# Kernel tuning notes

Measured on AMD Instinct MI355X. Metric: run time of the kernel, lower is better.

## Reference

```python
import jax, jax.numpy as jnp
import numpy as np

# Static pyramid shapes (H, W) per level; must match setup_inputs().
SPATIAL_SHAPES = [(128, 128), (64, 64), (32, 32), (16, 16)]
N, LQ, D_MODEL, M, L, P = 2, 21760, 256, 8, 4, 4
D_HEAD = D_MODEL // M
LEN_IN = sum(h * w for h, w in SPATIAL_SHAPES)


def _bilinear_sample(v, grid, H, W):
    """torch.grid_sample(mode=bilinear, padding=zeros, align_corners=False).
    v: [B, H, W, D], grid: [B, Q, P, 2] (x, y) in [-1, 1] -> [B, Q, P, D]."""
    gx = (grid[..., 0] + 1.0) * (W * 0.5) - 0.5
    gy = (grid[..., 1] + 1.0) * (H * 0.5) - 0.5
    x0 = jnp.floor(gx)
    y0 = jnp.floor(gy)
    wx1 = gx - x0
    wy1 = gy - y0
    b = jnp.arange(v.shape[0])[:, None, None]

    def gather(yi, xi):
        valid = (xi >= 0) & (xi <= W - 1) & (yi >= 0) & (yi <= H - 1)
        xc = jnp.clip(xi, 0, W - 1).astype(jnp.int32)
        yc = jnp.clip(yi, 0, H - 1).astype(jnp.int32)
        return v[b, yc, xc] * valid[..., None].astype(v.dtype)

    return (gather(y0, x0) * ((1 - wy1) * (1 - wx1))[..., None]
            + gather(y0, x0 + 1) * ((1 - wy1) * wx1)[..., None]
            + gather(y0 + 1, x0) * (wy1 * (1 - wx1))[..., None]
            + gather(y0 + 1, x0 + 1) * (wy1 * wx1)[..., None])


def setup_inputs() -> dict:
    key = jax.random.key(0)
    ks = jax.random.split(key, 12)
    s = 0.02
    return {
        "query": jax.random.normal(ks[0], (N, LQ, D_MODEL), jnp.float32),
        "reference_points": jax.random.uniform(ks[1], (N, LQ, L, 2), jnp.float32),
        "value": jax.random.normal(ks[2], (N, LEN_IN, D_MODEL), jnp.float32),
        "value_spatial_shapes": jnp.array(SPATIAL_SHAPES, jnp.int32),
        "W_val": jax.random.normal(ks[3], (D_MODEL, D_MODEL), jnp.float32) * s,
        "b_val": jnp.zeros((D_MODEL,), jnp.float32),
        "W_off": jax.random.normal(ks[4], (D_MODEL, M * L * P * 2), jnp.float32) * s,
        "b_off": jax.random.normal(ks[5], (M * L * P * 2,), jnp.float32) * s,
        "W_attn": jax.random.normal(ks[6], (D_MODEL, M * L * P), jnp.float32) * s,
        "b_attn": jnp.zeros((M * L * P,), jnp.float32),
        "W_out": jax.random.normal(ks[7], (D_MODEL, D_MODEL), jnp.float32) * s,
        "b_out": jnp.zeros((D_MODEL,), jnp.float32),
    }


def reference(query, reference_points, value, value_spatial_shapes,
              W_val, b_val, W_off, b_off, W_attn, b_attn, W_out, b_out):
    # value_spatial_shapes is treated as static (SPATIAL_SHAPES) for jit safety.
    v = (value @ W_val + b_val).reshape(N, LEN_IN, M, D_HEAD)
    off = (query @ W_off + b_off).reshape(N, LQ, M, L, P, 2)
    aw = jax.nn.softmax((query @ W_attn + b_attn).reshape(N, LQ, M, L * P), axis=-1)
    aw = aw.reshape(N, LQ, M, L, P)
    # normalizer stacks (W, H) -> x normalized by W, y by H
    norm = jnp.array([[w, h] for h, w in SPATIAL_SHAPES], dtype=query.dtype)
    loc = reference_points[:, :, None, :, None, :] + off / norm[None, None, None, :, None, :]
    grid = 2.0 * loc - 1.0  # [N, LQ, M, L, P, 2]

    out = jnp.zeros((N * M, LQ, D_HEAD), query.dtype)
    start = 0
    for lid, (H, W) in enumerate(SPATIAL_SHAPES):
        vl = v[:, start:start + H * W].reshape(N, H, W, M, D_HEAD)
        vl = vl.transpose(0, 3, 1, 2, 4).reshape(N * M, H, W, D_HEAD)
        gl = grid[:, :, :, lid].transpose(0, 2, 1, 3, 4).reshape(N * M, LQ, P, 2)
        sl = _bilinear_sample(vl, gl, H, W)  # [N*M, LQ, P, D]
        wl = aw[:, :, :, lid].transpose(0, 2, 1, 3).reshape(N * M, LQ, P)
        out = out + jnp.einsum('bqpd,bqp->bqd', sl, wl)
        start += H * W

    out = out.reshape(N, M, LQ, D_HEAD).transpose(0, 2, 1, 3).reshape(N, LQ, D_MODEL)
    return out @ W_out + b_out
```

## Files before the change

### kernel.cpp

```cpp
#include <hip/hip_runtime.h>

typedef __attribute__((ext_vector_type(8))) short short8;
typedef __attribute__((ext_vector_type(4))) float floatx4;

#define N_    2
#define LQ_   21760
#define D_    256
#define M_    8
#define L_    4
#define P_    4
#define DH_   32
#define LEN_  21760
#define BQ    16

__constant__ int c_start[4] = {0, 16384, 20480, 21504};
__constant__ int c_HW[4]    = {128, 64, 32, 16};

#define WT_BYTE_OFF 22282240u

__device__ __forceinline__ unsigned short f2bf(float f) {
  unsigned int u = __builtin_bit_cast(unsigned int, f);
  u += 0x7fffu + ((u >> 16) & 1u);
  return (unsigned short)(u >> 16);
}
__device__ __forceinline__ float bf2f(unsigned short s) {
  return __builtin_bit_cast(float, ((unsigned int)s) << 16);
}
__device__ __forceinline__ float bflo(unsigned int u) {
  return __builtin_bit_cast(float, u << 16);
}
__device__ __forceinline__ float bfhi(unsigned int u) {
  return __builtin_bit_cast(float, u & 0xffff0000u);
}

__global__ __launch_bounds__(256) void prep_kernel(
    const float* __restrict__ Woff, const float* __restrict__ Watt,
    const float* __restrict__ Wout, const float* __restrict__ Wv,
    unsigned short* __restrict__ wt) {
  const int b = blockIdx.x, t = threadIdx.x;
  const float* src; int ncols, n; unsigned short* dst;
  if (b < 256)      { src = Woff; ncols = 256; n = b;       dst = wt + 0      + n * 256; }
  else if (b < 384) { src = Watt; ncols = 128; n = b - 256; dst = wt + 65536  + n * 256; }
  else if (b < 640) { src = Wout; ncols = 256; n = b - 384; dst = wt + 98304  + n * 256; }
  else              { src = Wv;   ncols = 256; n = b - 640; dst = wt + 163840 + n * 256; }
  dst[t] = f2bf(src[(size_t)t * ncols + n]);
}

__global__ __launch_bounds__(256, 2) void vproj_kernel(
    const float* __restrict__ value, const unsigned short* __restrict__ Wvt,
    const float* __restrict__ bv, unsigned short* __restrict__ vout) {
  __shared__ unsigned short vs[64][264];
  const int t = threadIdx.x;
  const int r0 = blockIdx.x * 64;
  {
    const int c2 = (t & 127) * 2;
    const int rb = t >> 7;
#pragma unroll
    for (int i = 0; i < 32; ++i) {
      int rr = rb + i * 2;
      float2 v = *(const float2*)(value + (size_t)(r0 + rr) * D_ + c2);
      *(unsigned int*)&vs[rr][c2] = (unsigned int)f2bf(v.x) | ((unsigned int)f2bf(v.y) << 16);
    }
  }
  __syncthreads();
  const int wave = t >> 6, lane = t & 63;
  const int arow = wave * 16 + (lane & 15);
  const int kg = (lane >> 4) * 8;
  floatx4 acc[16] = {};
  for (int kk = 0; kk < 8; ++kk) {
    const int k0 = kk * 32;
    short8 af = *(const short8*)&vs[arow][k0 + kg];
#pragma unroll
    for (int ct = 0; ct < 16; ++ct) {
      const int col = ct * 16 + (lane & 15);
      short8 bf = *(const short8*)(Wvt + col * 256 + k0 + kg);
      acc[ct] = __builtin_amdgcn_mfma_f32_16x16x32_bf16(af, bf, acc[ct], 0, 0, 0);
    }
  }
  const int n = (r0 >= LEN_) ? 1 : 0;
  const int pixbase = r0 - n * LEN_ + wave * 16 + ((lane >> 4) * 4);
#pragma unroll
  for (int ct = 0; ct < 16; ++ct) {
    const int gc = ct * 16 + (lane & 15);
    const int m = gc >> 5, d = gc & 31;
    const float bb = bv[gc];
    unsigned short* ob = vout + ((size_t)(n * M_ + m) * LEN_) * DH_ + d;
#pragma unroll
    for (int j = 0; j < 4; ++j)
      ob[(size_t)(pixbase + j) * DH_] = f2bf(acc[ct][j] + bb);
  }
}

__global__ __launch_bounds__(256, 5)
__attribute__((amdgpu_waves_per_eu(4, 5)))
void msda_kernel(
    const float* __restrict__ query, const float* __restrict__ refp,
    const unsigned short* __restrict__ wt,
    const float* __restrict__ boff, const float* __restrict__ batt,
    const float* __restrict__ bout,
    const unsigned short* __restrict__ vproj, float* __restrict__ out) {
  __shared__ unsigned short qs[BQ][264];
  __shared__ unsigned short offb[BQ][256];
  __shared__ float awb[BQ][128];
  __shared__ short sidx[4][2][2][16];
  __shared__ float swls[4][2][2][16][4];

  const int t = threadIdx.x;
  const int lb = (blockIdx.x & 7) * 340 + (blockIdx.x >> 3);
  const int qg0 = lb * BQ;
  const int n = qg0 / LQ_;

  {
    const int c2 = (t & 127) * 2;
    const int rb = t >> 7;
#pragma unroll
    for (int i = 0; i < 8; ++i) {
      int rr = rb + i * 2;
      float2 v = *(const float2*)(query + (size_t)(qg0 + rr) * D_ + c2);
      *(unsigned int*)&qs[rr][c2] = (unsigned int)f2bf(v.x) | ((unsigned int)f2bf(v.y) << 16);
    }
  }
  __syncthreads();

  const int wave = t >> 6, lane = t & 63;
  const int arow = lane & 15;
  const int kg = (lane >> 4) * 8;
  const int row0 = (lane >> 4) * 4;

  {
    floatx4 acc[6] = {};
    for (int kk = 0; kk < 8; ++kk) {
      const int k0 = kk * 32;
      short8 af = *(const short8*)&qs[arow][k0 + kg];
#pragma unroll
      for (int i = 0; i < 6; ++i) {
        const int col = wave * 96 + i * 16 + (lane & 15);
        const unsigned short* bp = (col < 256) ? (wt + col * 256)
                                               : (wt + 65536 + (col - 256) * 256);
        short8 bf = *(const short8*)(bp + k0 + kg);
        acc[i] = __builtin_amdgcn_mfma_f32_16x16x32_bf16(af, bf, acc[i], 0, 0, 0);
      }
    }
#pragma unroll
    for (int i = 0; i < 6; ++i) {
      const int col = wave * 96 + i * 16 + (lane & 15);
      if (col < 256) {
        const float bb = boff[col];
#pragma unroll
        for (int j = 0; j < 4; ++j) offb[row0 + j][col] = f2bf(acc[i][j] + bb);
      } else {
        const float bb = batt[col - 256];
#pragma unroll
        for (int j = 0; j < 4; ++j) awb[row0 + j][col - 256] = acc[i][j] + bb;
      }
    }
  }
  __syncthreads();

  if (t < 128) {
    const int q = t >> 3, m = t & 7;
    float v[16]; float mx = -1e30f;
#pragma unroll
    for (int s = 0; s < 16; ++s) { v[s] = awb[q][m * 16 + s]; mx = fmaxf(mx, v[s]); }
    float sum = 0.f;
#pragma unroll
    for (int s = 0; s < 16; ++s) { v[s] = __expf(v[s] - mx); sum += v[s]; }
    const float inv = 1.f / sum;
#pragma unroll
    for (int s = 0; s < 16; ++s) awb[q][m * 16 + s] = v[s] * inv;
  }
  __syncthreads();

  const int qo  = lane >> 5;
  const int sh  = (lane >> 4) & 1;
  const int ss  = lane & 15;
  const int slv = ss >> 2;
  const int WlS = 128 >> slv;
  const int stS = c_start[slv];
  const int st_eq = (2 * wave + sh) * 16 + ss;
  const int hg = lane >> 5;
  const int m_g = 2 * wave + hg;
  const int g = lane & 31;
  const int sp = g >> 4, rsel = (g >> 3) & 1, csel = (g >> 2) & 1;
  const int wsel = (g >> 2) & 3, doct = g & 3;
  const char* vbyte = (const char*)vproj + (size_t)(n * M_ + m_g) * LEN_ * DH_ * 2;

  const float2* refp2 = (const float2*)refp;
  float2 rp[8];
#pragma unroll
  for (int e = 0; e < 8; ++e)
    rp[e] = refp2[(size_t)(qg0 + 2 * e + qo) * 4 + slv];

  for (int e = 0; e < 8; ++e) {
    {
      const int q = 2 * e + qo;
      const float gx = rp[e].x * (float)WlS + bf2f(offb[q][2 * st_eq])     - 0.5f;
      const float gy = rp[e].y * (float)WlS + bf2f(offb[q][2 * st_eq + 1]) - 0.5f;
      const float fx0 = floorf(gx), fy0 = floorf(gy);
      const int x0 = (int)fx0, y0 = (int)fy0;
      const float wx1 = gx - fx0, wy1 = gy - fy0;
      const float wx0 = 1.f - wx1, wy0 = 1.f - wy1;
      const float a = awb[q][st_eq];
      const bool vx0 = (x0 >= 0) && (x0 < WlS);
      const bool vx1 = (x0 + 1 >= 0) && (x0 + 1 < WlS);
      const bool vy0 = (y0 >= 0) && (y0 < WlS);
      const bool vy1 = (y0 + 1 >= 0) && (y0 + 1 < WlS);
      sidx[wave][qo][sh][ss] = (short)(stS + y0 * WlS + x0);
      swls[wave][qo][sh][ss][0] = (vy0 && vx0) ? wy0 * wx0 * a : 0.f;
      swls[wave][qo][sh][ss][1] = (vy0 && vx1) ? wy0 * wx1 * a : 0.f;
      swls[wave][qo][sh][ss][2] = (vy1 && vx0) ? wy1 * wx0 * a : 0.f;
      swls[wave][qo][sh][ss][3] = (vy1 && vx1) ? wy1 * wx1 * a : 0.f;
    }

#pragma unroll
    for (int qo2 = 0; qo2 < 2; ++qo2) {
      const int qp = 2 * e + qo2;
      uint4 u0, u1, u2, u3, u4, u5, u6, u7;
      float w0, w1, w2, w3, w4, w5, w6, w7;
#define GLD(i, WLC)                                                        \
      {                                                                    \
        const int s_ = 2 * (i) + sp;                                       \
        const int ix_ = (int)sidx[wave][qo2][hg][s_];                      \
        w##i = swls[wave][qo2][hg][s_][wsel];                              \
        int ofs_ = (ix_ + rsel * (WLC) + csel) * 64 + doct * 16;           \
        ofs_ = (ofs_ > 0) ? ofs_ : 0;                                      \
        u##i = *(const uint4*)(vbyte + ofs_);                              \
      }
      GLD(0, 128) GLD(1, 128) GLD(2, 64) GLD(3, 64)
      GLD(4, 32)  GLD(5, 32)  GLD(6, 16) GLD(7, 16)
#undef GLD

      float acc0 = 0.f, acc1 = 0.f, acc2 = 0.f, acc3 = 0.f;
      float acc4 = 0.f, acc5 = 0.f, acc6 = 0.f, acc7 = 0.f;
#define FMA8(i)                                                            \
      acc0 += bflo(u##i.x) * w##i; acc1 += bfhi(u##i.x) * w##i;            \
      acc2 += bflo(u##i.y) * w##i; acc3 += bfhi(u##i.y) * w##i;            \
      acc4 += bflo(u##i.z) * w##i; acc5 += bfhi(u##i.z) * w##i;            \
      acc6 += bflo(u##i.w) * w##i; acc7 += bfhi(u##i.w) * w##i;
      FMA8(0) FMA8(1) FMA8(2) FMA8(3) FMA8(4) FMA8(5) FMA8(6) FMA8(7)
#undef FMA8

      acc0 += __shfl_xor(acc0, 4);  acc1 += __shfl_xor(acc1, 4);
      acc2 += __shfl_xor(acc2, 4);  acc3 += __shfl_xor(acc3, 4);
      acc4 += __shfl_xor(acc4, 4);  acc5 += __shfl_xor(acc5, 4);
      acc6 += __shfl_xor(acc6, 4);  acc7 += __shfl_xor(acc7, 4);
      acc0 += __shfl_xor(acc0, 8);  acc1 += __shfl_xor(acc1, 8);
      acc2 += __shfl_xor(acc2, 8);  acc3 += __shfl_xor(acc3, 8);
      acc4 += __shfl_xor(acc4, 8);  acc5 += __shfl_xor(acc5, 8);
      acc6 += __shfl_xor(acc6, 8);  acc7 += __shfl_xor(acc7, 8);
      acc0 += __shfl_xor(acc0, 16); acc1 += __shfl_xor(acc1, 16);
      acc2 += __shfl_xor(acc2, 16); acc3 += __shfl_xor(acc3, 16);
      acc4 += __shfl_xor(acc4, 16); acc5 += __shfl_xor(acc5, 16);
      acc6 += __shfl_xor(acc6, 16); acc7 += __shfl_xor(acc7, 16);

      if (g < 4) {
        uint4 st4;
        st4.x = (unsigned int)f2bf(acc0) | ((unsigned int)f2bf(acc1) << 16);
        st4.y = (unsigned int)f2bf(acc2) | ((unsigned int)f2bf(acc3) << 16);
        st4.z = (unsigned int)f2bf(acc4) | ((unsigned int)f2bf(acc5) << 16);
        st4.w = (unsigned int)f2bf(acc6) | ((unsigned int)f2bf(acc7) << 16);
        *(uint4*)&qs[qp][m_g * 32 + doct * 8] = st4;
      }
    }
  }
  __syncthreads();

  {
    floatx4 acc[4] = {};
    for (int kk = 0; kk < 8; ++kk) {
      const int k0 = kk * 32;
      short8 af = *(const short8*)&qs[arow][k0 + kg];
#pragma unroll
      for (int i = 0; i < 4; ++i) {
        const int col = wave * 64 + i * 16 + (lane & 15);
        short8 bf = *(const short8*)(wt + 98304 + col * 256 + k0 + kg);
        acc[i] = __builtin_amdgcn_mfma_f32_16x16x32_bf16(af, bf, acc[i], 0, 0, 0);
      }
    }
#pragma unroll
    for (int i = 0; i < 4; ++i) {
      const int col = wave * 64 + i * 16 + (lane & 15);
      const float bb = bout[col];
#pragma unroll
      for (int j = 0; j < 4; ++j)
        out[(size_t)(qg0 + row0 + j) * D_ + col] = acc[i][j] + bb;
    }
  }
}

extern "C" void kernel_launch(void* const* d_in, const int* in_sizes, int n_in,
                              void* d_out, int out_size, void* d_ws, size_t ws_size,
                              hipStream_t stream) {
  const float* query = (const float*)d_in[0];
  const float* refp  = (const float*)d_in[1];
  const float* value = (const float*)d_in[2];
  const float* Wv    = (const float*)d_in[4];
  const float* bv    = (const float*)d_in[5];
  const float* Woff  = (const float*)d_in[6];
  const float* boff  = (const float*)d_in[7];
  const float* Watt  = (const float*)d_in[8];
  const float* batt  = (const float*)d_in[9];
  const float* Wout  = (const float*)d_in[10];
  const float* bout  = (const float*)d_in[11];
  float* out = (float*)d_out;

  unsigned short* vproj = (unsigned short*)d_ws;
  unsigned short* wt    = (unsigned short*)((char*)d_ws + WT_BYTE_OFF);
  const unsigned short* Wvt = wt + 163840;

  dim3 blk(256);
  hipLaunchKernelGGL(prep_kernel, dim3(896), blk, 0, stream, Woff, Watt, Wout, Wv, wt);
  hipLaunchKernelGGL(vproj_kernel, dim3((N_ * LEN_) / 64), blk, 0, stream, value, Wvt, bv, vproj);
  hipLaunchKernelGGL(msda_kernel, dim3((N_ * LQ_) / BQ), blk, 0, stream,
                     query, refp, wt, boff, batt, bout, vproj, out);
}
```

Baseline: 232.6 us.

## Split fused MSDA into per-head sampling kernel and separate output GEMM

Replaces the single fused msda kernel with two kernels when workspace allows. The first handles one (batch, head) pair per block over 64 queries, computing offsets and attention for that head only. Blocks are ordered by XCD so that each XCD's L2 cache serves a single head's value slice. It writes a bf16 intermediate, which a second MFMA kernel then multiplies by W_out. This aims for better cache locality in the gather, at the cost of an extra global round trip for the intermediate and one more launch.

```diff
diff --git a/kernel.cpp b/kernel.cpp
--- a/kernel.cpp
+++ b/kernel.cpp
@@ -17,6 +17,8 @@
 __constant__ int c_HW[4]    = {128, 64, 32, 16};
 
 #define WT_BYTE_OFF 22282240u
+#define MID_BYTE_OFF 22740992u
+#define WS_NEED_SPLIT 45023232ull
 
 __device__ __forceinline__ unsigned short f2bf(float f) {
   unsigned int u = __builtin_bit_cast(unsigned int, f);
@@ -88,6 +90,194 @@
 #pragma unroll
     for (int j = 0; j < 4; ++j)
       ob[(size_t)(pixbase + j) * DH_] = f2bf(acc[ct][j] + bb);
+  }
+}
+
+__global__ __launch_bounds__(256) void sample_kernel(
+    const float* __restrict__ query, const float* __restrict__ refp,
+    const unsigned short* __restrict__ wt,
+    const float* __restrict__ boff, const float* __restrict__ batt,
+    const unsigned short* __restrict__ vproj, unsigned short* __restrict__ mid) {
+  __shared__ unsigned short offh[64][34];
+  __shared__ float awh[64][17];
+  __shared__ short sidx[64][16];
+  __shared__ float swl[64][16][4];
+
+  const int t = threadIdx.x;
+  const int xcd = blockIdx.x & 7;
+  const int j = blockIdx.x >> 3;
+  const int pair = (j < 340) ? xcd : (8 + xcd);
+  const int qc = (j < 340) ? j : (j - 340);
+  const int n = pair >> 3, m = pair & 7;
+  const int q0 = qc * 64;
+  const size_t qrow0 = (size_t)n * LQ_ + q0;
+
+  const int wave = t >> 6, lane = t & 63;
+
+  {
+    const float* qptr = query + (qrow0 + wave * 16 + (lane & 15)) * D_;
+    floatx4 acc[3] = {};
+    for (int kk = 0; kk < 8; ++kk) {
+      const int k0 = kk * 32 + (lane >> 4) * 8;
+      float4 f0 = *(const float4*)(qptr + k0);
+      float4 f1 = *(const float4*)(qptr + k0 + 4);
+      short8 af;
+      af[0] = (short)f2bf(f0.x); af[1] = (short)f2bf(f0.y);
+      af[2] = (short)f2bf(f0.z); af[3] = (short)f2bf(f0.w);
+      af[4] = (short)f2bf(f1.x); af[5] = (short)f2bf(f1.y);
+      af[6] = (short)f2bf(f1.z); af[7] = (short)f2bf(f1.w);
+#pragma unroll
+      for (int i = 0; i < 3; ++i) {
+        const int lc = i * 16 + (lane & 15);
+        const unsigned short* bp = (lc < 32)
+            ? (wt + (m * 32 + lc) * 256)
+            : (wt + 65536 + (m * 16 + (lc - 32)) * 256);
+        short8 bf = *(const short8*)(bp + kk * 32 + (lane >> 4) * 8);
+        acc[i] = __builtin_amdgcn_mfma_f32_16x16x32_bf16(af, bf, acc[i], 0, 0, 0);
+      }
+    }
+    const int rw = wave * 16 + (lane >> 4) * 4;
+#pragma unroll
+    for (int i = 0; i < 3; ++i) {
+      const int lc = i * 16 + (lane & 15);
+      if (lc < 32) {
+        const float bb = boff[m * 32 + lc];
+#pragma unroll
+        for (int jj = 0; jj < 4; ++jj) offh[rw + jj][lc] = f2bf(acc[i][jj] + bb);
+      } else {
+        const float bb = batt[m * 16 + (lc - 32)];
+#pragma unroll
+        for (int jj = 0; jj < 4; ++jj) awh[rw + jj][lc - 32] = acc[i][jj] + bb;
+      }
+    }
+  }
+  __syncthreads();
+
+  if (t < 64) {
+    float v[16]; float mx = -1e30f;
+#pragma unroll
+    for (int s = 0; s < 16; ++s) { v[s] = awh[t][s]; mx = fmaxf(mx, v[s]); }
+    float sum = 0.f;
+#pragma unroll
+    for (int s = 0; s < 16; ++s) { v[s] = __expf(v[s] - mx); sum += v[s]; }
+    const float inv = 1.f / sum;
+#pragma unroll
+    for (int s = 0; s < 16; ++s) awh[t][s] = v[s] * inv;
+  }
+  __syncthreads();
+
+  {
+    const int q = t >> 2;
+    const int l = t & 3;
+    const int Wl = 128 >> l;
+    const int st = c_start[l];
+    const float2 rpv = *(const float2*)(refp + ((qrow0 + q) * 4 + l) * 2);
+#pragma unroll
+    for (int jj = 0; jj < 4; ++jj) {
+      const int s = l * 4 + jj;
+      const float gx = rpv.x * (float)Wl + bf2f(offh[q][2 * s])     - 0.5f;
+      const float gy = rpv.y * (float)Wl + bf2f(offh[q][2 * s + 1]) - 0.5f;
+      const float fx0 = floorf(gx), fy0 = floorf(gy);
+      const int x0 = (int)fx0, y0 = (int)fy0;
+      const float wx1 = gx - fx0, wy1 = gy - fy0;
+      const float wx0 = 1.f - wx1, wy0 = 1.f - wy1;
+      const float a = awh[q][s];
+      const bool vx0 = (x0 >= 0) && (x0 < Wl);
+      const bool vx1 = (x0 + 1 >= 0) && (x0 + 1 < Wl);
+      const bool vy0 = (y0 >= 0) && (y0 < Wl);
+      const bool vy1 = (y0 + 1 >= 0) && (y0 + 1 < Wl);
+      sidx[q][s] = (short)(st + y0 * Wl + x0);
+      swl[q][s][0] = (vy0 && vx0) ? wy0 * wx0 * a : 0.f;
+      swl[q][s][1] = (vy0 && vx1) ? wy0 * wx1 * a : 0.f;
+      swl[q][s][2] = (vy1 && vx0) ? wy1 * wx0 * a : 0.f;
+      swl[q][s][3] = (vy1 && vx1) ? wy1 * wx1 * a : 0.f;
+    }
+  }
+  __syncthreads();
+
+  const int qo = lane >> 5;
+  const int g = lane & 31;
+  const int sp = g >> 4, rsel = (g >> 3) & 1, csel = (g >> 2) & 1;
+  const int wsel = (g >> 2) & 3, doct = g & 3;
+  const char* vbyte = (const char*)vproj + (size_t)(n * M_ + m) * LEN_ * DH_ * 2;
+
+  for (int it = 0; it < 8; ++it) {
+    const int q = wave * 16 + it * 2 + qo;
+    uint4 u0, u1, u2, u3, u4, u5, u6, u7;
+    float w0, w1, w2, w3, w4, w5, w6, w7;
+#define GLD(i, WLC)                                                        \
+    {                                                                      \
+      const int s_ = 2 * (i) + sp;                                         \
+      const int ix_ = (int)sidx[q][s_];                                    \
+      w##i = swl[q][s_][wsel];                                             \
+      int ofs_ = (ix_ + rsel * (WLC) + csel) * 64 + doct * 16;             \
+      ofs_ = (ofs_ > 0) ? ofs_ : 0;                                        \
+      u##i = *(const uint4*)(vbyte + ofs_);                                \
+    }
+    GLD(0, 128) GLD(1, 128) GLD(2, 64) GLD(3, 64)
+    GLD(4, 32)  GLD(5, 32)  GLD(6, 16) GLD(7, 16)
+#undef GLD
+
+    float acc0 = 0.f, acc1 = 0.f, acc2 = 0.f, acc3 = 0.f;
+    float acc4 = 0.f, acc5 = 0.f, acc6 = 0.f, acc7 = 0.f;
+#define FMA8(i)                                                            \
+    acc0 += bflo(u##i.x) * w##i; acc1 += bfhi(u##i.x) * w##i;              \
+    acc2 += bflo(u##i.y) * w##i; acc3 += bfhi(u##i.y) * w##i;              \
+    acc4 += bflo(u##i.z) * w##i; acc5 += bfhi(u##i.z) * w##i;              \
+    acc6 += bflo(u##i.w) * w##i; acc7 += bfhi(u##i.w) * w##i;
+    FMA8(0) FMA8(1) FMA8(2) FMA8(3) FMA8(4) FMA8(5) FMA8(6) FMA8(7)
+#undef FMA8
+
+    acc0 += __shfl_xor(acc0, 4);  acc1 += __shfl_xor(acc1, 4);
+    acc2 += __shfl_xor(acc2, 4);  acc3 += __shfl_xor(acc3, 4);
+    acc4 += __shfl_xor(acc4, 4);  acc5 += __shfl_xor(acc5, 4);
+    acc6 += __shfl_xor(acc6, 4);  acc7 += __shfl_xor(acc7, 4);
+    acc0 += __shfl_xor(acc0, 8);  acc1 += __shfl_xor(acc1, 8);
+    acc2 += __shfl_xor(acc2, 8);  acc3 += __shfl_xor(acc3, 8);
+    acc4 += __shfl_xor(acc4, 8);  acc5 += __shfl_xor(acc5, 8);
+    acc6 += __shfl_xor(acc6, 8);  acc7 += __shfl_xor(acc7, 8);
+    acc0 += __shfl_xor(acc0, 16); acc1 += __shfl_xor(acc1, 16);
+    acc2 += __shfl_xor(acc2, 16); acc3 += __shfl_xor(acc3, 16);
+    acc4 += __shfl_xor(acc4, 16); acc5 += __shfl_xor(acc5, 16);
+    acc6 += __shfl_xor(acc6, 16); acc7 += __shfl_xor(acc7, 16);
+
+    if (g < 4) {
+      uint4 st4;
+      st4.x = (unsigned int)f2bf(acc0) | ((unsigned int)f2bf(acc1) << 16);
+      st4.y = (unsigned int)f2bf(acc2) | ((unsigned int)f2bf(acc3) << 16);
+      st4.z = (unsigned int)f2bf(acc4) | ((unsigned int)f2bf(acc5) << 16);
+      st4.w = (unsigned int)f2bf(acc6) | ((unsigned int)f2bf(acc7) << 16);
+      *(uint4*)(mid + ((qrow0 + q) * 8 + m) * 32 + doct * 8) = st4;
+    }
+  }
+}
+
+__global__ __launch_bounds__(256, 2) void outgemm_kernel(
+    const unsigned short* __restrict__ mid, const unsigned short* __restrict__ wtout,
+    const float* __restrict__ bout, float* __restrict__ out) {
+  const int t = threadIdx.x;
+  const int r0 = blockIdx.x * 64;
+  const int wave = t >> 6, lane = t & 63;
+  const int arow = r0 + wave * 16 + (lane & 15);
+  const int kg = (lane >> 4) * 8;
+  floatx4 acc[16] = {};
+  for (int kk = 0; kk < 8; ++kk) {
+    short8 af = *(const short8*)(mid + (size_t)arow * 256 + kk * 32 + kg);
+#pragma unroll
+    for (int ct = 0; ct < 16; ++ct) {
+      const int col = ct * 16 + (lane & 15);
+      short8 bf = *(const short8*)(wtout + col * 256 + kk * 32 + kg);
+      acc[ct] = __builtin_amdgcn_mfma_f32_16x16x32_bf16(af, bf, acc[ct], 0, 0, 0);
+    }
+  }
+  const int rwb = r0 + wave * 16 + (lane >> 4) * 4;
+#pragma unroll
+  for (int ct = 0; ct < 16; ++ct) {
+    const int col = ct * 16 + (lane & 15);
+    const float bb = bout[col];
+#pragma unroll
+    for (int jd = 0; jd < 4; ++jd)
+      out[(size_t)(rwb + jd) * D_ + col] = acc[ct][jd] + bb;
   }
 }
 
@@ -311,6 +501,15 @@
   dim3 blk(256);
   hipLaunchKernelGGL(prep_kernel, dim3(896), blk, 0, stream, Woff, Watt, Wout, Wv, wt);
   hipLaunchKernelGGL(vproj_kernel, dim3((N_ * LEN_) / 64), blk, 0, stream, value, Wvt, bv, vproj);
-  hipLaunchKernelGGL(msda_kernel, dim3((N_ * LQ_) / BQ), blk, 0, stream,
-                     query, refp, wt, boff, batt, bout, vproj, out);
-}
+
+  if (ws_size >= WS_NEED_SPLIT) {
+    unsigned short* mid = (unsigned short*)((char*)d_ws + MID_BYTE_OFF);
+    hipLaunchKernelGGL(sample_kernel, dim3(5440), blk, 0, stream,
+                       query, refp, wt, boff, batt, vproj, mid);
+    hipLaunchKernelGGL(outgemm_kernel, dim3((N_ * LQ_) / 64), blk, 0, stream,
+                       mid, wt + 98304, bout, out);
+  } else {
+    hipLaunchKernelGGL(msda_kernel, dim3((N_ * LQ_) / BQ), blk, 0, stream,
+                       query, refp, wt, boff, batt, bout, vproj, out);
+  }
+}
```

Result: slower. 266.5 us (+14.6%).

## Software-pipeline sampling setup with batched gathers and lower occupancy target

Applied to the files above, without the earlier changes.

Restructures the per-query sampling loop so all 16 value gathers for both queries are issued together. The next iteration's coordinate and weight setup is computed before the loads are consumed, with sched_barriers to keep that ordering. Occupancy hints drop from 5 to 4 waves per EU, freeing registers for the extra in-flight loads. This should hide gather latency better. Risks: the per-wave shared sidx/swls buffers are overwritten by the next setup while the current values are already held in registers, and the lower occupancy may reduce latency hiding across waves.

```diff
diff --git a/kernel.cpp b/kernel.cpp
--- a/kernel.cpp
+++ b/kernel.cpp
@@ -31,6 +31,15 @@
 }
 __device__ __forceinline__ float bfhi(unsigned int u) {
   return __builtin_bit_cast(float, u & 0xffff0000u);
+}
+
+__device__ __forceinline__ void fma8v(const uint4 u, const float w,
+    float& a0, float& a1, float& a2, float& a3,
+    float& a4, float& a5, float& a6, float& a7) {
+  a0 += bflo(u.x) * w; a1 += bfhi(u.x) * w;
+  a2 += bflo(u.y) * w; a3 += bfhi(u.y) * w;
+  a4 += bflo(u.z) * w; a5 += bfhi(u.z) * w;
+  a6 += bflo(u.w) * w; a7 += bfhi(u.w) * w;
 }
 
 __global__ __launch_bounds__(256) void prep_kernel(
@@ -91,8 +100,7 @@
   }
 }
 
-__global__ __launch_bounds__(256, 5)
-__attribute__((amdgpu_waves_per_eu(4, 5)))
+__global__ __launch_bounds__(256, 4)
 void msda_kernel(
     const float* __restrict__ query, const float* __restrict__ refp,
     const unsigned short* __restrict__ wt,
@@ -186,83 +194,97 @@
   const char* vbyte = (const char*)vproj + (size_t)(n * M_ + m_g) * LEN_ * DH_ * 2;
 
   const float2* refp2 = (const float2*)refp;
-  float2 rp[8];
-#pragma unroll
-  for (int e = 0; e < 8; ++e)
-    rp[e] = refp2[(size_t)(qg0 + 2 * e + qo) * 4 + slv];
+
+#define SETUP(EP)                                                            \
+  {                                                                          \
+    const int q_ = 2 * (EP) + qo;                                            \
+    const float2 rpv = refp2[(size_t)(qg0 + q_) * 4 + slv];                  \
+    const float gx = rpv.x * (float)WlS + bf2f(offb[q_][2 * st_eq]) - 0.5f;  \
+    const float gy = rpv.y * (float)WlS + bf2f(offb[q_][2 * st_eq + 1]) - 0.5f; \
+    const float fx0 = floorf(gx), fy0 = floorf(gy);                          \
+    const int x0 = (int)fx0, y0 = (int)fy0;                                  \
+    const float wx1 = gx - fx0, wy1 = gy - fy0;                              \
+    const float wx0 = 1.f - wx1, wy0 = 1.f - wy1;                            \
+    const float a = awb[q_][st_eq];                                          \
+    const bool vx0 = (x0 >= 0) && (x0 < WlS);                                \
+    const bool vx1 = (x0 + 1 >= 0) && (x0 + 1 < WlS);                        \
+    const bool vy0 = (y0 >= 0) && (y0 < WlS);                                \
+    const bool vy1 = (y0 + 1 >= 0) && (y0 + 1 < WlS);                        \
+    sidx[wave][qo][sh][ss] = (short)(stS + y0 * WlS + x0);                   \
+    swls[wave][qo][sh][ss][0] = (vy0 && vx0) ? wy0 * wx0 * a : 0.f;          \
+    swls[wave][qo][sh][ss][1] = (vy0 && vx1) ? wy0 * wx1 * a : 0.f;          \
+    swls[wave][qo][sh][ss][2] = (vy1 && vx0) ? wy1 * wx0 * a : 0.f;          \
+    swls[wave][qo][sh][ss][3] = (vy1 && vx1) ? wy1 * wx1 * a : 0.f;          \
+  }
+
+  SETUP(0)
 
   for (int e = 0; e < 8; ++e) {
-    {
-      const int q = 2 * e + qo;
-      const float gx = rp[e].x * (float)WlS + bf2f(offb[q][2 * st_eq])     - 0.5f;
-      const float gy = rp[e].y * (float)WlS + bf2f(offb[q][2 * st_eq + 1]) - 0.5f;
-      const float fx0 = floorf(gx), fy0 = floorf(gy);
-      const int x0 = (int)fx0, y0 = (int)fy0;
-      const float wx1 = gx - fx0, wy1 = gy - fy0;
-      const float wx0 = 1.f - wx1, wy0 = 1.f - wy1;
-      const float a = awb[q][st_eq];
-      const bool vx0 = (x0 >= 0) && (x0 < WlS);
-      const bool vx1 = (x0 + 1 >= 0) && (x0 + 1 < WlS);
-      const bool vy0 = (y0 >= 0) && (y0 < WlS);
-      const bool vy1 = (y0 + 1 >= 0) && (y0 + 1 < WlS);
-      sidx[wave][qo][sh][ss] = (short)(stS + y0 * WlS + x0);
-      swls[wave][qo][sh][ss][0] = (vy0 && vx0) ? wy0 * wx0 * a : 0.f;
-      swls[wave][qo][sh][ss][1] = (vy0 && vx1) ? wy0 * wx1 * a : 0.f;
-      swls[wave][qo][sh][ss][2] = (vy1 && vx0) ? wy1 * wx0 * a : 0.f;
-      swls[wave][qo][sh][ss][3] = (vy1 && vx1) ? wy1 * wx1 * a : 0.f;
-    }
-
-#pragma unroll
-    for (int qo2 = 0; qo2 < 2; ++qo2) {
-      const int qp = 2 * e + qo2;
-      uint4 u0, u1, u2, u3, u4, u5, u6, u7;
-      float w0, w1, w2, w3, w4, w5, w6, w7;
-#define GLD(i, WLC)                                                        \
-      {                                                                    \
-        const int s_ = 2 * (i) + sp;                                       \
-        const int ix_ = (int)sidx[wave][qo2][hg][s_];                      \
-        w##i = swls[wave][qo2][hg][s_][wsel];                              \
-        int ofs_ = (ix_ + rsel * (WLC) + csel) * 64 + doct * 16;           \
-        ofs_ = (ofs_ > 0) ? ofs_ : 0;                                      \
-        u##i = *(const uint4*)(vbyte + ofs_);                              \
-      }
-      GLD(0, 128) GLD(1, 128) GLD(2, 64) GLD(3, 64)
-      GLD(4, 32)  GLD(5, 32)  GLD(6, 16) GLD(7, 16)
+    const short* ipA = &sidx[wave][0][hg][0];
+    const short* ipB = &sidx[wave][1][hg][0];
+    const float* wpA = &swls[wave][0][hg][0][wsel];
+    const float* wpB = &swls[wave][1][hg][0][wsel];
+    uint4 uA0, uA1, uA2, uA3, uA4, uA5, uA6, uA7;
+    uint4 uB0, uB1, uB2, uB3, uB4, uB5, uB6, uB7;
+    float wA0, wA1, wA2, wA3, wA4, wA5, wA6, wA7;
+    float wB0, wB1, wB2, wB3, wB4, wB5, wB6, wB7;
+#define GLD(P, i, WLC)                                                       \
+    {                                                                        \
+      const int s_ = 2 * (i) + sp;                                           \
+      const int ix_ = (int)ip##P[s_];                                        \
+      w##P##i = wp##P[s_ * 4];                                               \
+      int ofs_ = (ix_ + rsel * (WLC) + csel) * 64 + doct * 16;               \
+      ofs_ = (ofs_ > 0) ? ofs_ : 0;                                          \
+      u##P##i = *(const uint4*)(vbyte + ofs_);                               \
+    }
+    GLD(A, 0, 128) GLD(A, 1, 128) GLD(A, 2, 64) GLD(A, 3, 64)
+    GLD(A, 4, 32)  GLD(A, 5, 32)  GLD(A, 6, 16) GLD(A, 7, 16)
+    GLD(B, 0, 128) GLD(B, 1, 128) GLD(B, 2, 64) GLD(B, 3, 64)
+    GLD(B, 4, 32)  GLD(B, 5, 32)  GLD(B, 6, 16) GLD(B, 7, 16)
 #undef GLD
-
-      float acc0 = 0.f, acc1 = 0.f, acc2 = 0.f, acc3 = 0.f;
-      float acc4 = 0.f, acc5 = 0.f, acc6 = 0.f, acc7 = 0.f;
-#define FMA8(i)                                                            \
-      acc0 += bflo(u##i.x) * w##i; acc1 += bfhi(u##i.x) * w##i;            \
-      acc2 += bflo(u##i.y) * w##i; acc3 += bfhi(u##i.y) * w##i;            \
-      acc4 += bflo(u##i.z) * w##i; acc5 += bfhi(u##i.z) * w##i;            \
-      acc6 += bflo(u##i.w) * w##i; acc7 += bfhi(u##i.w) * w##i;
-      FMA8(0) FMA8(1) FMA8(2) FMA8(3) FMA8(4) FMA8(5) FMA8(6) FMA8(7)
-#undef FMA8
-
-      acc0 += __shfl_xor(acc0, 4);  acc1 += __shfl_xor(acc1, 4);
-      acc2 += __shfl_xor(acc2, 4);  acc3 += __shfl_xor(acc3, 4);
-      acc4 += __shfl_xor(acc4, 4);  acc5 += __shfl_xor(acc5, 4);
-      acc6 += __shfl_xor(acc6, 4);  acc7 += __shfl_xor(acc7, 4);
-      acc0 += __shfl_xor(acc0, 8);  acc1 += __shfl_xor(acc1, 8);
-      acc2 += __shfl_xor(acc2, 8);  acc3 += __shfl_xor(acc3, 8);
-      acc4 += __shfl_xor(acc4, 8);  acc5 += __shfl_xor(acc5, 8);
-      acc6 += __shfl_xor(acc6, 8);  acc7 += __shfl_xor(acc7, 8);
-      acc0 += __shfl_xor(acc0, 16); acc1 += __shfl_xor(acc1, 16);
-      acc2 += __shfl_xor(acc2, 16); acc3 += __shfl_xor(acc3, 16);
-      acc4 += __shfl_xor(acc4, 16); acc5 += __shfl_xor(acc5, 16);
-      acc6 += __shfl_xor(acc6, 16); acc7 += __shfl_xor(acc7, 16);
-
-      if (g < 4) {
-        uint4 st4;
-        st4.x = (unsigned int)f2bf(acc0) | ((unsigned int)f2bf(acc1) << 16);
-        st4.y = (unsigned int)f2bf(acc2) | ((unsigned int)f2bf(acc3) << 16);
-        st4.z = (unsigned int)f2bf(acc4) | ((unsigned int)f2bf(acc5) << 16);
-        st4.w = (unsigned int)f2bf(acc6) | ((unsigned int)f2bf(acc7) << 16);
-        *(uint4*)&qs[qp][m_g * 32 + doct * 8] = st4;
-      }
-    }
-  }
+    __builtin_amdgcn_sched_barrier(0);
+
+    if (e < 7) SETUP(e + 1)
+    __builtin_amdgcn_sched_barrier(0);
+
+#define CONSUME(P, QP)                                                       \
+    {                                                                        \
+      float acc0 = 0.f, acc1 = 0.f, acc2 = 0.f, acc3 = 0.f;                  \
+      float acc4 = 0.f, acc5 = 0.f, acc6 = 0.f, acc7 = 0.f;                  \
+      fma8v(u##P##0, w##P##0, acc0, acc1, acc2, acc3, acc4, acc5, acc6, acc7); \
+      fma8v(u##P##1, w##P##1, acc0, acc1, acc2, acc3, acc4, acc5, acc6, acc7); \
+      fma8v(u##P##2, w##P##2, acc0, acc1, acc2, acc3, acc4, acc5, acc6, acc7); \
+      fma8v(u##P##3, w##P##3, acc0, acc1, acc2, acc3, acc4, acc5, acc6, acc7); \
+      fma8v(u##P##4, w##P##4, acc0, acc1, acc2, acc3, acc4, acc5, acc6, acc7); \
+      fma8v(u##P##5, w##P##5, acc0, acc1, acc2, acc3, acc4, acc5, acc6, acc7); \
+      fma8v(u##P##6, w##P##6, acc0, acc1, acc2, acc3, acc4, acc5, acc6, acc7); \
+      fma8v(u##P##7, w##P##7, acc0, acc1, acc2, acc3, acc4, acc5, acc6, acc7); \
+      acc0 += __shfl_xor(acc0, 4);  acc1 += __shfl_xor(acc1, 4);             \
+      acc2 += __shfl_xor(acc2, 4);  acc3 += __shfl_xor(acc3, 4);             \
+      acc4 += __shfl_xor(acc4, 4);  acc5 += __shfl_xor(acc5, 4);             \
+      acc6 += __shfl_xor(acc6, 4);  acc7 += __shfl_xor(acc7, 4);             \
+      acc0 += __shfl_xor(acc0, 8);  acc1 += __shfl_xor(acc1, 8);             \
+      acc2 += __shfl_xor(acc2, 8);  acc3 += __shfl_xor(acc3, 8);             \
+      acc4 += __shfl_xor(acc4, 8);  acc5 += __shfl_xor(acc5, 8);             \
+      acc6 += __shfl_xor(acc6, 8);  acc7 += __shfl_xor(acc7, 8);             \
+      acc0 += __shfl_xor(acc0, 16); acc1 += __shfl_xor(acc1, 16);            \
+      acc2 += __shfl_xor(acc2, 16); acc3 += __shfl_xor(acc3, 16);            \
+      acc4 += __shfl_xor(acc4, 16); acc5 += __shfl_xor(acc5, 16);            \
+      acc6 += __shfl_xor(acc6, 16); acc7 += __shfl_xor(acc7, 16);            \
+      if (g < 4) {                                                           \
+        uint4 st4;                                                           \
+        st4.x = (unsigned int)f2bf(acc0) | ((unsigned int)f2bf(acc1) << 16); \
+        st4.y = (unsigned int)f2bf(acc2) | ((unsigned int)f2bf(acc3) << 16); \
+        st4.z = (unsigned int)f2bf(acc4) | ((unsigned int)f2bf(acc5) << 16); \
+        st4.w = (unsigned int)f2bf(acc6) | ((unsigned int)f2bf(acc7) << 16); \
+        *(uint4*)&qs[QP][m_g * 32 + doct * 8] = st4;                         \
+      }                                                                      \
+    }
+    CONSUME(A, 2 * e)
+    CONSUME(B, 2 * e + 1)
+#undef CONSUME
+  }
+#undef SETUP
   __syncthreads();
 
   {
```

New measurement: 241.5 us. +3.8%, slower.
